# Performance work log

Hardware: AMD Instinct MI355X
Metric: run time of the kernel (lower is better)

Reference implementation:

```python
import jax, jax.numpy as jnp
import numpy as np

N_HEADS = 16

def setup_inputs() -> dict:
    key = jax.random.key(0)
    ks = jax.random.split(key, 5)
    B, T, C = 4, 2048, 1024
    scale = 0.02
    return {
        "x": jax.random.normal(ks[0], (B, T, C), dtype=jnp.float32),
        "w_qkv": jax.random.normal(ks[1], (C, 3 * C), dtype=jnp.float32) * scale,
        "b_qkv": jax.random.normal(ks[2], (3 * C,), dtype=jnp.float32) * scale,
        "w_out": jax.random.normal(ks[3], (C, C), dtype=jnp.float32) * scale,
        "b_out": jax.random.normal(ks[4], (C,), dtype=jnp.float32) * scale,
    }

def reference(x, w_qkv, b_qkv, w_out, b_out):
    B, T, C = x.shape
    H = N_HEADS
    D = C // H
    scale = 1.0 / jnp.sqrt(jnp.asarray(D, x.dtype))
    qkv = x @ w_qkv + b_qkv                       # (B,T,3C)
    q, k, v = jnp.split(qkv, 3, axis=-1)
    q = q.reshape(B, T, H, D).transpose(0, 2, 1, 3)  # (B,H,T,D)
    k = k.reshape(B, T, H, D).transpose(0, 2, 1, 3)
    v = v.reshape(B, T, H, D).transpose(0, 2, 1, 3)
    att = jnp.einsum("bhqd,bhkd->bhqk", q, k) * scale  # (B,H,T,T)
    causal = jnp.tril(jnp.ones((T, T), dtype=bool))
    att = jnp.where(causal[None, None], att, -jnp.inf)
    att = jax.nn.softmax(att, axis=-1)
    y = jnp.einsum("bhqk,bhkd->bhqd", att, v)     # (B,H,T,D)
    y = y.transpose(0, 2, 1, 3).reshape(B, T, C)
    return y @ w_out + b_out
```

## Files before the change

### kernel.cpp

```cpp
#include <hip/hip_runtime.h>
#include <hip/hip_bf16.h>

typedef __bf16 bf16;
typedef __attribute__((__ext_vector_type__(4))) __bf16 bf16x4;
typedef __attribute__((__ext_vector_type__(8))) __bf16 bf16x8;
typedef __attribute__((__ext_vector_type__(4))) float f32x4;

#define MFMA16(a, b, c) __builtin_amdgcn_mfma_f32_16x16x32_bf16(a, b, c, 0, 0, 0)

static __device__ __forceinline__ bf16 f2b(float f) { return (bf16)f; }

static __device__ __forceinline__ void gload16(const void* g, void* l) {
    __builtin_amdgcn_global_load_lds(
        (const __attribute__((address_space(1))) int*)g,
        (__attribute__((address_space(3))) int*)l, 16, 0, 0);
}

__global__ __launch_bounds__(256) void xcast(
    const float* __restrict__ in, bf16* __restrict__ out)
{
    size_t i = ((size_t)blockIdx.x * 256 + threadIdx.x) * 16;
    float4 a0 = *(const float4*)(in + i);
    float4 a1 = *(const float4*)(in + i + 4);
    float4 a2 = *(const float4*)(in + i + 8);
    float4 a3 = *(const float4*)(in + i + 12);
    bf16x8 p0, p1;
    p0[0] = f2b(a0.x); p0[1] = f2b(a0.y); p0[2] = f2b(a0.z); p0[3] = f2b(a0.w);
    p0[4] = f2b(a1.x); p0[5] = f2b(a1.y); p0[6] = f2b(a1.z); p0[7] = f2b(a1.w);
    p1[0] = f2b(a2.x); p1[1] = f2b(a2.y); p1[2] = f2b(a2.z); p1[3] = f2b(a2.w);
    p1[4] = f2b(a3.x); p1[5] = f2b(a3.y); p1[6] = f2b(a3.z); p1[7] = f2b(a3.w);
    *(bf16x8*)(out + i) = p0;
    *(bf16x8*)(out + i + 8) = p1;
}

__global__ __launch_bounds__(256) void cast_transpose(
    const float* __restrict__ in, bf16* __restrict__ out, int R, int Cc)
{
    __shared__ float tile[32][33];
    const int c0 = blockIdx.x * 32, r0 = blockIdx.y * 32;
    const int tx = threadIdx.x & 31, ty = threadIdx.x >> 5;
#pragma unroll
    for (int i = ty; i < 32; i += 8)
        tile[i][tx] = in[(size_t)(r0 + i) * Cc + c0 + tx];
    __syncthreads();
#pragma unroll
    for (int i = ty; i < 32; i += 8)
        out[(size_t)(c0 + i) * R + r0 + tx] = f2b(tile[tx][i]);
}

#define QSCALE (0.125f * 1.44269504f)

__global__ __launch_bounds__(256) void qkv_gemm(
    const bf16* __restrict__ Xb, const bf16* __restrict__ Wt,
    const float* __restrict__ bias,
    bf16* __restrict__ Qb, bf16* __restrict__ Kb, bf16* __restrict__ Vt)
{
    __shared__ __align__(16) bf16 As[128 * 32];
    __shared__ __align__(16) bf16 Bs[128 * 32];
    const int m0 = blockIdx.x * 128, n0 = blockIdx.y * 128;
    const int tid = threadIdx.x, lane = tid & 63, w = tid >> 6;
    const int wr = (w >> 1) * 64, wc = (w & 1) * 64;
    const int lg = lane >> 4, lr = lane & 15;
    const int srow = tid >> 2, scol = (tid & 3) * 8;
    f32x4 acc[4][4] = {};

    for (int k0 = 0; k0 < 1024; k0 += 32) {
#pragma unroll
        for (int half = 0; half < 2; ++half) {
            const int r = srow + half * 64;
            gload16(Xb + (size_t)(m0 + r) * 1024 + k0 + scol,
                    As + half * 2048 + w * 512);
            gload16(Wt + (size_t)(n0 + r) * 1024 + k0 + scol,
                    Bs + half * 2048 + w * 512);
        }
        __syncthreads();

        bf16x8 af[4], bfr[4];
#pragma unroll
        for (int m = 0; m < 4; ++m)
            af[m] = *(const bf16x8*)(As + (wr + m * 16 + lr) * 32 + lg * 8);
#pragma unroll
        for (int n = 0; n < 4; ++n)
            bfr[n] = *(const bf16x8*)(Bs + (wc + n * 16 + lr) * 32 + lg * 8);
#pragma unroll
        for (int m = 0; m < 4; ++m)
#pragma unroll
            for (int n = 0; n < 4; ++n)
                acc[m][n] = MFMA16(af[m], bfr[n], acc[m][n]);
        __syncthreads();
    }

#pragma unroll
    for (int m = 0; m < 4; ++m)
#pragma unroll
        for (int n = 0; n < 4; ++n) {
            int gn = n0 + wc + n * 16 + lr;
            int which = gn >> 10, cc = gn & 1023;
            int h = cc >> 6, d = cc & 63;
            float bv = bias[gn];
            if (which == 2) {
                int gm0 = m0 + wr + m * 16 + lg * 4;
                int b = gm0 >> 11, t0 = gm0 & 2047;
                size_t bh = (size_t)(b * 16 + h);
                bf16x4 pk;
#pragma unroll
                for (int j = 0; j < 4; ++j) pk[j] = f2b(acc[m][n][j] + bv);
                *(bf16x4*)(Vt + (bh * 64 + d) * 2048 + t0) = pk;
            } else {
#pragma unroll
                for (int j = 0; j < 4; ++j) {
                    int gm = m0 + wr + m * 16 + lg * 4 + j;
                    int b = gm >> 11, t = gm & 2047;
                    size_t bh = (size_t)(b * 16 + h);
                    if (which == 0)
                        Qb[(bh * 2048 + t) * 64 + d] =
                            f2b((acc[m][n][j] + bv) * QSCALE);
                    else
                        Kb[(bh * 2048 + t) * 64 + d] = f2b(acc[m][n][j] + bv);
                }
            }
        }
}

__global__ __launch_bounds__(256, 6) void attn(
    const bf16* __restrict__ Qb, const bf16* __restrict__ Kb,
    const bf16* __restrict__ Vt, bf16* __restrict__ Yb)
{
    __shared__ __align__(16) bf16 Ks[64 * 64];
    __shared__ __align__(16) bf16 Vs[64 * 64];
    __shared__ __align__(16) bf16 Ps[4][16 * 64];
    const int lid = blockIdx.x;
    const int xcd = lid & 7, idx = lid >> 3;
    const int bh = xcd * 8 + (idx >> 5);
    const int qi = idx & 31;
    const int q0 = qi * 64;
    const int tid = threadIdx.x, lane = tid & 63, w = tid >> 6;
    const int lg = lane >> 4, lr = lane & 15;

    const bf16* qr = Qb + ((size_t)bh * 2048 + q0 + w * 16 + lr) * 64;
    bf16x8 qf0 = *(const bf16x8*)(qr + lg * 8);
    bf16x8 qf1 = *(const bf16x8*)(qr + 32 + lg * 8);

    const bf16 one = (bf16)1.0f;
    const bf16x8 vones = {one, one, one, one, one, one, one, one};

    f32x4 o[4] = {};
    f32x4 oL = {};

    const int sr = tid >> 2;
    const int c0 = (tid & 3) * 2;
    const int sp = c0 * 8;
    const int d0 = sr * 64 + ((c0 ^ (sr & 7)) << 3);
    const int d1 = sr * 64 + (((c0 + 1) ^ (sr & 7)) << 3);
    const int swa = ((lg ^ (lr & 7)) << 3);
    const int swb = (((lg + 4) ^ (lr & 7)) << 3);
    const int pbase = lr * 64 + (lg & 1) * 4;

    auto sm = [&](f32x4 (&s)[4], bool diag, bf16x8& pf0, bf16x8& pf1) {
        if (diag) {
            const int qloc = w * 16 + lr;
#pragma unroll
            for (int n = 0; n < 4; ++n)
#pragma unroll
                for (int j = 0; j < 4; ++j)
                    if (n * 16 + lg * 4 + j > qloc) s[n][j] = -1e30f;
        }
#pragma unroll
        for (int n = 0; n < 4; ++n) {
            bf16x4 pk;
#pragma unroll
            for (int j = 0; j < 4; ++j)
                pk[j] = f2b(exp2f(s[n][j]));
            *(bf16x4*)(&Ps[w][pbase + (((n * 2 + (lg >> 1)) ^ (lr & 7)) << 3)]) = pk;
        }
        pf0 = *(const bf16x8*)(&Ps[w][lr * 64 + swa]);
        pf1 = *(const bf16x8*)(&Ps[w][lr * 64 + swb]);
    };

    const int ntiles = qi + 1;
    for (int it = 0; it < ntiles; ++it) {
        const int j0 = it * 64;
        const bf16* ksrc = Kb + ((size_t)bh * 2048 + j0 + sr) * 64 + sp;
        int4 k0r = *(const int4*)ksrc;
        int4 k1r = *(const int4*)(ksrc + 8);
        const bf16* vsrc = Vt + ((size_t)bh * 64 + sr) * 2048 + j0 + sp;
        int4 v0r = *(const int4*)vsrc;
        int4 v1r = *(const int4*)(vsrc + 8);
        *(int4*)(Ks + d0) = k0r;
        *(int4*)(Ks + d1) = k1r;
        *(int4*)(Vs + d0) = v0r;
        *(int4*)(Vs + d1) = v1r;
        __syncthreads();

        f32x4 s[4];
        __builtin_amdgcn_s_setprio(1);
#pragma unroll
        for (int n = 0; n < 4; ++n) {
            const bf16* krow = Ks + (n * 16 + lr) * 64;
            bf16x8 kf0 = *(const bf16x8*)(krow + swa);
            bf16x8 kf1 = *(const bf16x8*)(krow + swb);
            f32x4 z = {};
            z = MFMA16(kf0, qf0, z);
            z = MFMA16(kf1, qf1, z);
            s[n] = z;
        }
        __builtin_amdgcn_s_setprio(0);

        bf16x8 pf0, pf1;
        sm(s, it == qi, pf0, pf1);

        __builtin_amdgcn_s_setprio(1);
        oL = MFMA16(pf0, vones, oL);
        oL = MFMA16(pf1, vones, oL);
#pragma unroll
        for (int n = 0; n < 4; ++n) {
            const bf16* vrow = Vs + (n * 16 + lr) * 64;
            bf16x8 vf0 = *(const bf16x8*)(vrow + swa);
            bf16x8 vf1 = *(const bf16x8*)(vrow + swb);
            o[n] = MFMA16(pf0, vf0, o[n]);
            o[n] = MFMA16(pf1, vf1, o[n]);
        }
        __builtin_amdgcn_s_setprio(0);
        __syncthreads();
    }

    const int b = bh >> 4, h = bh & 15;
    float lj[4];
#pragma unroll
    for (int j = 0; j < 4; ++j) lj[j] = 1.f / oL[j];
#pragma unroll
    for (int n = 0; n < 4; ++n)
#pragma unroll
        for (int j = 0; j < 4; ++j) {
            int qr2 = q0 + w * 16 + lg * 4 + j;
            Yb[((size_t)b * 2048 + qr2) * 1024 + h * 64 + n * 16 + lr] =
                f2b(o[n][j] * lj[j]);
        }
}

__global__ __launch_bounds__(256) void out_gemm(
    const bf16* __restrict__ Y, const bf16* __restrict__ Wt,
    const float* __restrict__ bias, float* __restrict__ Out)
{
    __shared__ __align__(16) bf16 As[128 * 32];
    __shared__ __align__(16) bf16 Bs[128 * 32];
    const int m0 = blockIdx.x * 128, n0 = blockIdx.y * 128;
    const int tid = threadIdx.x, lane = tid & 63, w = tid >> 6;
    const int wr = (w >> 1) * 64, wc = (w & 1) * 64;
    const int lg = lane >> 4, lr = lane & 15;
    const int srow = tid >> 2, scol = (tid & 3) * 8;
    f32x4 acc[4][4] = {};

    for (int k0 = 0; k0 < 1024; k0 += 32) {
#pragma unroll
        for (int half = 0; half < 2; ++half) {
            const int r = srow + half * 64;
            gload16(Y  + (size_t)(m0 + r) * 1024 + k0 + scol,
                    As + half * 2048 + w * 512);
            gload16(Wt + (size_t)(n0 + r) * 1024 + k0 + scol,
                    Bs + half * 2048 + w * 512);
        }
        __syncthreads();

        bf16x8 af[4], bfr[4];
#pragma unroll
        for (int m = 0; m < 4; ++m)
            af[m] = *(const bf16x8*)(As + (wr + m * 16 + lr) * 32 + lg * 8);
#pragma unroll
        for (int n = 0; n < 4; ++n)
            bfr[n] = *(const bf16x8*)(Bs + (wc + n * 16 + lr) * 32 + lg * 8);
#pragma unroll
        for (int m = 0; m < 4; ++m)
#pragma unroll
            for (int n = 0; n < 4; ++n)
                acc[m][n] = MFMA16(af[m], bfr[n], acc[m][n]);
        __syncthreads();
    }

#pragma unroll
    for (int m = 0; m < 4; ++m)
#pragma unroll
        for (int n = 0; n < 4; ++n)
#pragma unroll
            for (int j = 0; j < 4; ++j) {
                int gm = m0 + wr + m * 16 + lg * 4 + j;
                int gn = n0 + wc + n * 16 + lr;
                Out[(size_t)gm * 1024 + gn] = acc[m][n][j] + bias[gn];
            }
}

extern "C" void kernel_launch(void* const* d_in, const int* in_sizes, int n_in,
                              void* d_out, int out_size, void* d_ws, size_t ws_size,
                              hipStream_t stream)
{
    const float* x     = (const float*)d_in[0];
    const float* w_qkv = (const float*)d_in[1];
    const float* b_qkv = (const float*)d_in[2];
    const float* w_out = (const float*)d_in[3];
    const float* b_out = (const float*)d_in[4];
    float* out = (float*)d_out;

    char* ws = (char*)d_ws;
    bf16* wqkvT = (bf16*)(ws);
    bf16* woutT = (bf16*)(ws + 6291456);
    bf16* Qb    = (bf16*)(ws + 6291456 + 2097152);
    bf16* Kb    = (bf16*)(ws + 6291456 + 2097152 + 16777216);
    bf16* Vt    = (bf16*)(ws + 6291456 + 2097152 + 2u * 16777216u);
    bf16* Xb    = (bf16*)(ws + 6291456 + 2097152 + 3u * 16777216u);
    bf16* Yb    = Xb;

    xcast<<<2048, 256, 0, stream>>>(x, Xb);
    cast_transpose<<<dim3(96, 32), 256, 0, stream>>>(w_qkv, wqkvT, 1024, 3072);
    cast_transpose<<<dim3(32, 32), 256, 0, stream>>>(w_out, woutT, 1024, 1024);
    qkv_gemm<<<dim3(64, 24), 256, 0, stream>>>(Xb, wqkvT, b_qkv, Qb, Kb, Vt);
    attn<<<2048, 256, 0, stream>>>(Qb, Kb, Vt, Yb);
    out_gemm<<<dim3(64, 8), 256, 0, stream>>>(Yb, woutT, b_out, out);
}
```

Measured before the change: 188.0 us.

## Pair complementary causal query tiles per attention block to balance work and share K/V

Each attention block now has 512 threads in two 4-wave groups, handling query tile ia and its complement 31-ia. K/V tiles are loaded once into shared memory and reused by both groups, so every block does the same total causal work and per-tile K/V loads are shared. The group with the shorter tile stays idle, but still hits the barriers, for the last iterations. This costs some wave-level idleness and doubles the block size, in exchange for less load imbalance across blocks and less global K/V traffic.

Result: no change. 187.0 us (-0.5%).

```diff
diff --git a/kernel.cpp b/kernel.cpp
--- a/kernel.cpp
+++ b/kernel.cpp
@@ -122,22 +122,26 @@
         }
 }
 
-__global__ __launch_bounds__(256, 6) void attn(
+__global__ __launch_bounds__(512, 8) void attn(
     const bf16* __restrict__ Qb, const bf16* __restrict__ Kb,
     const bf16* __restrict__ Vt, bf16* __restrict__ Yb)
 {
     __shared__ __align__(16) bf16 Ks[64 * 64];
     __shared__ __align__(16) bf16 Vs[64 * 64];
-    __shared__ __align__(16) bf16 Ps[4][16 * 64];
+    __shared__ __align__(16) bf16 Ps[8][16 * 64];
     const int lid = blockIdx.x;
     const int xcd = lid & 7, idx = lid >> 3;
-    const int bh = xcd * 8 + (idx >> 5);
-    const int qi = idx & 31;
-    const int q0 = qi * 64;
+    const int bh = xcd * 8 + (idx >> 4);
+    const int pair = idx & 15;
+    const int ia = pair, ib = 31 - pair;
     const int tid = threadIdx.x, lane = tid & 63, w = tid >> 6;
+    const int g = w >> 2;
+    const int wl = w & 3;
+    const int qt = g ? ia : ib;
+    const int q0w = qt * 64;
     const int lg = lane >> 4, lr = lane & 15;
 
-    const bf16* qr = Qb + ((size_t)bh * 2048 + q0 + w * 16 + lr) * 64;
+    const bf16* qr = Qb + ((size_t)bh * 2048 + q0w + wl * 16 + lr) * 64;
     bf16x8 qf0 = *(const bf16x8*)(qr + lg * 8);
     bf16x8 qf1 = *(const bf16x8*)(qr + 32 + lg * 8);
 
@@ -147,18 +151,17 @@
     f32x4 o[4] = {};
     f32x4 oL = {};
 
-    const int sr = tid >> 2;
-    const int c0 = (tid & 3) * 2;
-    const int sp = c0 * 8;
-    const int d0 = sr * 64 + ((c0 ^ (sr & 7)) << 3);
-    const int d1 = sr * 64 + (((c0 + 1) ^ (sr & 7)) << 3);
+    const int srow = tid >> 3;
+    const int sc = tid & 7;
+    const int sp = sc * 8;
+    const int dst = srow * 64 + ((sc ^ (srow & 7)) << 3);
     const int swa = ((lg ^ (lr & 7)) << 3);
     const int swb = (((lg + 4) ^ (lr & 7)) << 3);
     const int pbase = lr * 64 + (lg & 1) * 4;
 
     auto sm = [&](f32x4 (&s)[4], bool diag, bf16x8& pf0, bf16x8& pf1) {
         if (diag) {
-            const int qloc = w * 16 + lr;
+            const int qloc = wl * 16 + lr;
 #pragma unroll
             for (int n = 0; n < 4; ++n)
 #pragma unroll
@@ -177,50 +180,47 @@
         pf1 = *(const bf16x8*)(&Ps[w][lr * 64 + swb]);
     };
 
-    const int ntiles = qi + 1;
+    const int ntiles = ib + 1;
     for (int it = 0; it < ntiles; ++it) {
         const int j0 = it * 64;
-        const bf16* ksrc = Kb + ((size_t)bh * 2048 + j0 + sr) * 64 + sp;
-        int4 k0r = *(const int4*)ksrc;
-        int4 k1r = *(const int4*)(ksrc + 8);
-        const bf16* vsrc = Vt + ((size_t)bh * 64 + sr) * 2048 + j0 + sp;
-        int4 v0r = *(const int4*)vsrc;
-        int4 v1r = *(const int4*)(vsrc + 8);
-        *(int4*)(Ks + d0) = k0r;
-        *(int4*)(Ks + d1) = k1r;
-        *(int4*)(Vs + d0) = v0r;
-        *(int4*)(Vs + d1) = v1r;
-        __syncthreads();
-
-        f32x4 s[4];
-        __builtin_amdgcn_s_setprio(1);
-#pragma unroll
-        for (int n = 0; n < 4; ++n) {
-            const bf16* krow = Ks + (n * 16 + lr) * 64;
-            bf16x8 kf0 = *(const bf16x8*)(krow + swa);
-            bf16x8 kf1 = *(const bf16x8*)(krow + swb);
-            f32x4 z = {};
-            z = MFMA16(kf0, qf0, z);
-            z = MFMA16(kf1, qf1, z);
-            s[n] = z;
-        }
-        __builtin_amdgcn_s_setprio(0);
-
-        bf16x8 pf0, pf1;
-        sm(s, it == qi, pf0, pf1);
-
-        __builtin_amdgcn_s_setprio(1);
-        oL = MFMA16(pf0, vones, oL);
-        oL = MFMA16(pf1, vones, oL);
-#pragma unroll
-        for (int n = 0; n < 4; ++n) {
-            const bf16* vrow = Vs + (n * 16 + lr) * 64;
-            bf16x8 vf0 = *(const bf16x8*)(vrow + swa);
-            bf16x8 vf1 = *(const bf16x8*)(vrow + swb);
-            o[n] = MFMA16(pf0, vf0, o[n]);
-            o[n] = MFMA16(pf1, vf1, o[n]);
-        }
-        __builtin_amdgcn_s_setprio(0);
+        int4 kr = *(const int4*)(Kb + ((size_t)bh * 2048 + j0 + srow) * 64 + sp);
+        int4 vr = *(const int4*)(Vt + ((size_t)bh * 64 + srow) * 2048 + j0 + sp);
+        *(int4*)(Ks + dst) = kr;
+        *(int4*)(Vs + dst) = vr;
+        __syncthreads();
+
+        const bool active = (g == 0) || (it <= ia);
+        if (active) {
+            f32x4 s[4];
+            __builtin_amdgcn_s_setprio(1);
+#pragma unroll
+            for (int n = 0; n < 4; ++n) {
+                const bf16* krow = Ks + (n * 16 + lr) * 64;
+                bf16x8 kf0 = *(const bf16x8*)(krow + swa);
+                bf16x8 kf1 = *(const bf16x8*)(krow + swb);
+                f32x4 z = {};
+                z = MFMA16(kf0, qf0, z);
+                z = MFMA16(kf1, qf1, z);
+                s[n] = z;
+            }
+            __builtin_amdgcn_s_setprio(0);
+
+            bf16x8 pf0, pf1;
+            sm(s, it == qt, pf0, pf1);
+
+            __builtin_amdgcn_s_setprio(1);
+            oL = MFMA16(pf0, vones, oL);
+            oL = MFMA16(pf1, vones, oL);
+#pragma unroll
+            for (int n = 0; n < 4; ++n) {
+                const bf16* vrow = Vs + (n * 16 + lr) * 64;
+                bf16x8 vf0 = *(const bf16x8*)(vrow + swa);
+                bf16x8 vf1 = *(const bf16x8*)(vrow + swb);
+                o[n] = MFMA16(pf0, vf0, o[n]);
+                o[n] = MFMA16(pf1, vf1, o[n]);
+            }
+            __builtin_amdgcn_s_setprio(0);
+        }
         __syncthreads();
     }
 
@@ -232,7 +232,7 @@
     for (int n = 0; n < 4; ++n)
 #pragma unroll
         for (int j = 0; j < 4; ++j) {
-            int qr2 = q0 + w * 16 + lg * 4 + j;
+            int qr2 = q0w + wl * 16 + lg * 4 + j;
             Yb[((size_t)b * 2048 + qr2) * 1024 + h * 64 + n * 16 + lr] =
                 f2b(o[n][j] * lj[j]);
         }
@@ -313,6 +313,6 @@
     cast_transpose<<<dim3(96, 32), 256, 0, stream>>>(w_qkv, wqkvT, 1024, 3072);
     cast_transpose<<<dim3(32, 32), 256, 0, stream>>>(w_out, woutT, 1024, 1024);
     qkv_gemm<<<dim3(64, 24), 256, 0, stream>>>(Xb, wqkvT, b_qkv, Qb, Kb, Vt);
-    attn<<<2048, 256, 0, stream>>>(Qb, Kb, Vt, Yb);
+    attn<<<1024, 512, 0, stream>>>(Qb, Kb, Vt, Yb);
     out_gemm<<<dim3(64, 8), 256, 0, stream>>>(Yb, woutT, b_out, out);
 }
```
